# Performance work log

Measured on AMD Instinct MI355X. Metric: run time of the kernel, lower is better.

The kernel has to match this reference:

```python
import jax, jax.numpy as jnp
import numpy as np

H, C, DK = 4, 63, 64   # n_head, context_size, d_k
NF = H * DK            # n_feat = 256


def setup_inputs() -> dict:
    key = jax.random.key(0)
    ks = jax.random.split(key, 7)
    B, T = 2, 4096
    query = jax.random.normal(ks[0], (B, T, NF), jnp.float32)
    key_t = jax.random.normal(ks[1], (B, T, NF), jnp.float32)   # dummy, unused
    value = jax.random.normal(ks[2], (B, T, NF), jnp.float32)
    mask = jnp.ones((B, 1, T), jnp.bool_)                       # dummy, unused
    s = 1.0 / np.sqrt(NF).astype(np.float32)
    w1 = jax.random.normal(ks[3], (NF, NF), jnp.float32) * s
    w2 = jax.random.normal(ks[4], (H * C, NF), jnp.float32) * s
    w3 = jax.random.normal(ks[5], (NF, NF), jnp.float32) * s
    w_out = jax.random.normal(ks[6], (NF, NF), jnp.float32) * s
    return {"query": query, "key": key_t, "value": value, "mask": mask,
            "w1": w1, "w2": w2, "w3": w3, "w_out": w_out}


def reference(query, key, value, mask, w1, w2, w3, w_out):
    # key and mask are dummies (unused), matching the original module.
    B, T, _ = query.shape
    half = (C - 1) // 2

    q = query @ w1.T                                            # (B,T,NF)
    # synthesized band scores: (B,H,T,C)
    weight = (jax.nn.relu(q) @ w2.T).reshape(B, T, H, C).transpose(0, 2, 1, 3)

    # band geometry: score(i, j) lives at offset k = j - i + half, |j-i| <= half
    j_idx = jnp.arange(T)[:, None] + jnp.arange(C)[None, :] - half   # (T,C)
    valid = (j_idx >= 0) & (j_idx < T)                               # (T,C)
    scores = jnp.where(valid[None, None], weight, -jnp.inf)
    p_attn = jax.nn.softmax(scores, axis=-1)                         # (B,H,T,C)

    v = (value @ w3.T).reshape(B, T, H, DK).transpose(0, 2, 1, 3)    # (B,H,T,DK)
    jc = jnp.clip(j_idx, 0, T - 1)                                   # safe gather idx
    windows = v[:, :, jc, :]                                         # (B,H,T,C,DK)
    x = jnp.einsum('bhtc,bhtcd->bhtd', p_attn, windows)              # (B,H,T,DK)

    x = x.transpose(0, 2, 1, 3).reshape(B, T, NF)
    return x @ w_out.T
```

## Files before the change

### kernel.cpp

```cpp
#include <hip/hip_runtime.h>
#include <hip/hip_bf16.h>
#include <math.h>

typedef _Float16 f16x8 __attribute__((ext_vector_type(8)));
typedef _Float16 f16x4 __attribute__((ext_vector_type(4)));
typedef float    f32x4 __attribute__((ext_vector_type(4)));

__device__ __host__ __forceinline__ int swz(int ch, int row) {
    return (ch & 24) | ((ch & 7) ^ (row & 7));
}
__device__ __forceinline__ f32x4 mfma16(f16x8 a, f16x8 b, f32x4 c) {
    return __builtin_amdgcn_mfma_f32_16x16x32_f16(a, b, c, 0, 0, 0);
}
__device__ __forceinline__ f16x8 cvt8(float4 lo, float4 hi) {
    f16x8 r = { (_Float16)lo.x, (_Float16)lo.y, (_Float16)lo.z, (_Float16)lo.w,
                (_Float16)hi.x, (_Float16)hi.y, (_Float16)hi.z, (_Float16)hi.w };
    return r;
}

__global__ __launch_bounds__(256) void convw(const float* __restrict__ w1,
                                             const float* __restrict__ w2,
                                             const float* __restrict__ w3,
                                             const float* __restrict__ wo,
                                             _Float16* __restrict__ p1,
                                             _Float16* __restrict__ p2,
                                             _Float16* __restrict__ p3,
                                             _Float16* __restrict__ po) {
    int gid = blockIdx.x * 256 + threadIdx.x;
    int widx = gid >> 13;
    int r    = gid & 8191;
    int lane = r & 63;
    int ks   = (r >> 6) & 7;
    int nblk = r >> 9;
    int n  = nblk * 16 + (lane & 15);
    int kc = (ks * 4 + (lane >> 4)) * 8;
    const float* src = widx == 0 ? w1 : widx == 1 ? w2 : widx == 2 ? w3 : wo;
    _Float16*    dst = widx == 0 ? p1 : widx == 1 ? p2 : widx == 2 ? p3 : po;
    f16x8 h = {};
    if (!(widx == 1 && n >= 252)) {
        float4 lo = *(const float4*)&src[n * 256 + kc];
        float4 hi = *(const float4*)&src[n * 256 + kc + 4];
        h = cvt8(lo, hi);
    }
    *(f16x8*)&dst[r * 8] = h;
}

__global__ __launch_bounds__(1024) void mono(const float* __restrict__ query,
                                             const float* __restrict__ value,
                                             const _Float16* __restrict__ w1p,
                                             const _Float16* __restrict__ w2p,
                                             const _Float16* __restrict__ w3p,
                                             const _Float16* __restrict__ wop,
                                             float* __restrict__ outp) {
    __shared__ __align__(16) _Float16 RA[16384];
    __shared__ __align__(16) _Float16 RB[8192];
    __shared__ __align__(16) _Float16 Vs[24576];
    __shared__ __align__(16) _Float16 vwT[26624];

    const int tid = threadIdx.x, lane = tid & 63, wid = tid >> 6;
    const int bidr = blockIdx.x;
    const int work = (bidr & 7) * 32 + (bidr >> 3);
    const int b   = work >> 7;
    const int t0  = (work & 127) * 32;
    const size_t rowb = (size_t)b * 4096;

    _Float16* Aq = RA;
    _Float16* Qr = RA + 8192;
    _Float16* Pl = RA;
    _Float16* sc = RB;
    _Float16* xb = RB;

    {
        int row = tid >> 5, ch = tid & 31;
        const float* p = &query[(rowb + t0 + row) * 256 + ch * 8];
        float4 lo = *(const float4*)p, hi = *(const float4*)(p + 4);
        *(f16x8*)&Aq[row * 256 + swz(ch, row) * 8] = cvt8(lo, hi);
    }
    #pragma unroll
    for (int it = 0; it < 3; ++it) {
        int slot = it * 1024 + tid;
        int row = slot >> 5, ch = slot & 31;
        int jl = t0 - 32 + row;
        jl = jl < 0 ? 0 : (jl > 4095 ? 4095 : jl);
        const float* p = &value[(rowb + jl) * 256 + ch * 8];
        float4 lo = *(const float4*)p, hi = *(const float4*)(p + 4);
        *(f16x8*)&Vs[row * 256 + swz(ch, row) * 8] = cvt8(lo, hi);
    }
    __syncthreads();

    const int wm = wid >> 3;
    const int wn = wid & 7;

    {
        f32x4 acc[2] = {};
        #pragma unroll
        for (int ks = 0; ks < 8; ++ks) {
            int chn = ks * 4 + (lane >> 4);
            int row = wm * 16 + (lane & 15);
            f16x8 af = *(const f16x8*)&Aq[row * 256 + swz(chn, row) * 8];
            #pragma unroll
            for (int j = 0; j < 2; ++j) {
                f16x8 bf = *(const f16x8*)&w1p[(((wn * 2 + j) * 8 + ks) * 64 + lane) * 8];
                acc[j] = mfma16(af, bf, acc[j]);
            }
        }
        #pragma unroll
        for (int j = 0; j < 2; ++j)
            #pragma unroll
            for (int r = 0; r < 4; ++r) {
                int row = wm * 16 + ((lane >> 4) << 2) + r;
                int n   = wn * 32 + j * 16 + (lane & 15);
                float v = fmaxf(acc[j][r], 0.f);
                Qr[row * 256 + swz(n >> 3, row) * 8 + (n & 7)] = (_Float16)v;
            }
    }
    __syncthreads();

    {
        f32x4 acc[2] = {};
        #pragma unroll
        for (int ks = 0; ks < 8; ++ks) {
            int chn = ks * 4 + (lane >> 4);
            int row = wm * 16 + (lane & 15);
            f16x8 af = *(const f16x8*)&Qr[row * 256 + swz(chn, row) * 8];
            #pragma unroll
            for (int j = 0; j < 2; ++j) {
                f16x8 bf = *(const f16x8*)&w2p[(((wn * 2 + j) * 8 + ks) * 64 + lane) * 8];
                acc[j] = mfma16(af, bf, acc[j]);
            }
        }
        #pragma unroll
        for (int j = 0; j < 2; ++j)
            #pragma unroll
            for (int r = 0; r < 4; ++r) {
                int row = wm * 16 + ((lane >> 4) << 2) + r;
                int n   = wn * 32 + j * 16 + (lane & 15);
                sc[row * 256 + n] = (_Float16)acc[j][r];
            }
    }

    {
        f32x4 a3[3][2] = {};
        #pragma unroll
        for (int ks = 0; ks < 8; ++ks) {
            int chn = ks * 4 + (lane >> 4);
            f16x8 bf[2];
            #pragma unroll
            for (int j = 0; j < 2; ++j)
                bf[j] = *(const f16x8*)&w3p[(((wn * 2 + j) * 8 + ks) * 64 + lane) * 8];
            #pragma unroll
            for (int mi = 0; mi < 3; ++mi) {
                int row = (wm * 3 + mi) * 16 + (lane & 15);
                f16x8 af = *(const f16x8*)&Vs[row * 256 + swz(chn, row) * 8];
                #pragma unroll
                for (int j = 0; j < 2; ++j)
                    a3[mi][j] = mfma16(af, bf[j], a3[mi][j]);
            }
        }
        #pragma unroll
        for (int mi = 0; mi < 3; ++mi)
            #pragma unroll
            for (int j = 0; j < 2; ++j) {
                int d  = wn * 32 + j * 16 + (lane & 15);
                int jw = (wm * 3 + mi) * 16 + ((lane >> 4) << 2);
                f16x4 h = { (_Float16)a3[mi][j][0], (_Float16)a3[mi][j][1],
                            (_Float16)a3[mi][j][2], (_Float16)a3[mi][j][3] };
                *(f16x4*)&vwT[d * 104 + jw] = h;
            }
    }
    __syncthreads();

    const int h = wid >> 2, q = wid & 3;
    #pragma unroll
    for (int it = 0; it < 2; ++it) {
        int s = it * 64 + lane;
        if (s < 104) {
            int rr = h * 32 + q * 8 + s / 13;
            int cc = s % 13;
            f16x8 z = {};
            *(f16x8*)&Pl[rr * 104 + cc * 8] = z;
        }
    }

    {
        const int hf = lane >> 5, c = lane & 31;
        #pragma unroll
        for (int i = 0; i < 4; ++i) {
            int tl = q * 8 + 2 * i + hf;
            int t  = t0 + tl;
            int c1 = c + 32;
            int j0 = t + c - 31, j1 = t + c1 - 31;
            bool ok0 = (j0 >= 0) && (j0 < 4096);
            bool ok1 = (c1 < 63) && (j1 >= 0) && (j1 < 4096);
            float s0 = ok0 ? (float)sc[tl * 256 + h * 63 + c]  : -INFINITY;
            float s1 = ok1 ? (float)sc[tl * 256 + h * 63 + c1] : -INFINITY;
            float mx = fmaxf(s0, s1);
            #pragma unroll
            for (int off = 16; off > 0; off >>= 1) mx = fmaxf(mx, __shfl_xor(mx, off));
            float e0 = ok0 ? __expf(s0 - mx) : 0.f;
            float e1 = ok1 ? __expf(s1 - mx) : 0.f;
            float sum = e0 + e1;
            #pragma unroll
            for (int off = 16; off > 0; off >>= 1) sum += __shfl_xor(sum, off);
            float inv = 1.0f / sum;
            Pl[(h * 32 + tl) * 104 + (tl + c + 1)] = (_Float16)(e0 * inv);
            if (c1 < 63) Pl[(h * 32 + tl) * 104 + (tl + c1 + 1)] = (_Float16)(e1 * inv);
        }
    }
    __syncthreads();

    {
        const int th = (wid >> 1) & 1, dh = wid & 1;
        f32x4 xa[2] = {};
        #pragma unroll
        for (int ks = 0; ks < 3; ++ks) {
            int chn = ks * 4 + (lane >> 4);
            f16x8 af = *(const f16x8*)&Pl[(h * 32 + th * 16 + (lane & 15)) * 104 + chn * 8];
            #pragma unroll
            for (int j = 0; j < 2; ++j) {
                f16x8 bf = *(const f16x8*)&vwT[(h * 64 + dh * 32 + j * 16 + (lane & 15)) * 104 + chn * 8];
                xa[j] = mfma16(af, bf, xa[j]);
            }
        }
        #pragma unroll
        for (int j = 0; j < 2; ++j)
            #pragma unroll
            for (int r = 0; r < 4; ++r) {
                int row = th * 16 + ((lane >> 4) << 2) + r;
                int n   = h * 64 + dh * 32 + j * 16 + (lane & 15);
                xb[row * 256 + swz(n >> 3, row) * 8 + (n & 7)] = (_Float16)xa[j][r];
            }
    }
    __syncthreads();

    {
        f32x4 oa[2] = {};
        #pragma unroll
        for (int ks = 0; ks < 8; ++ks) {
            int chn = ks * 4 + (lane >> 4);
            int row = wm * 16 + (lane & 15);
            f16x8 af = *(const f16x8*)&xb[row * 256 + swz(chn, row) * 8];
            #pragma unroll
            for (int j = 0; j < 2; ++j) {
                f16x8 bf = *(const f16x8*)&wop[(((wn * 2 + j) * 8 + ks) * 64 + lane) * 8];
                oa[j] = mfma16(af, bf, oa[j]);
            }
        }
        #pragma unroll
        for (int j = 0; j < 2; ++j)
            #pragma unroll
            for (int r = 0; r < 4; ++r) {
                int m = t0 + wm * 16 + ((lane >> 4) << 2) + r;
                int n = wn * 32 + j * 16 + (lane & 15);
                outp[(rowb + m) * 256 + n] = oa[j][r];
            }
    }
}

extern "C" void kernel_launch(void* const* d_in, const int* in_sizes, int n_in,
                              void* d_out, int out_size, void* d_ws, size_t ws_size,
                              hipStream_t stream) {
    const float* query = (const float*)d_in[0];
    const float* value = (const float*)d_in[2];
    const float* w1    = (const float*)d_in[4];
    const float* w2    = (const float*)d_in[5];
    const float* w3    = (const float*)d_in[6];
    const float* w_out = (const float*)d_in[7];

    char* ws = (char*)d_ws;
    _Float16* w1p = (_Float16*)ws;
    _Float16* w2p = w1p + 65536;
    _Float16* w3p = w2p + 65536;
    _Float16* wop = w3p + 65536;

    convw<<<dim3(128), dim3(256), 0, stream>>>(w1, w2, w3, w_out, w1p, w2p, w3p, wop);
    mono<<<dim3(256), dim3(1024), 0, stream>>>(query, value, w1p, w2p, w3p, wop, (float*)d_out);
}
```

Baseline: 28.69 us.

## Repartition GEMM warps by output column and preload weight fragments

Each of the 16 waves now owns a 16-column slice of every GEMM's output across all rows, instead of a 2x8 grid of row and column tiles. Each wave therefore loads its weight fragments from global memory once into registers up front, and those fragments are reused across the row tiles. The global loads for query and value are all issued before their conversions and shared-memory stores, so the latency overlaps. Launch bounds now give a min-blocks hint, and the change raises register pressure from the eight preloaded fragments.

```diff
diff --git a/kernel.cpp b/kernel.cpp
--- a/kernel.cpp
+++ b/kernel.cpp
@@ -45,13 +45,13 @@
     *(f16x8*)&dst[r * 8] = h;
 }
 
-__global__ __launch_bounds__(1024) void mono(const float* __restrict__ query,
-                                             const float* __restrict__ value,
-                                             const _Float16* __restrict__ w1p,
-                                             const _Float16* __restrict__ w2p,
-                                             const _Float16* __restrict__ w3p,
-                                             const _Float16* __restrict__ wop,
-                                             float* __restrict__ outp) {
+__global__ __launch_bounds__(1024, 4) void mono(const float* __restrict__ query,
+                                                const float* __restrict__ value,
+                                                const _Float16* __restrict__ w1p,
+                                                const _Float16* __restrict__ w2p,
+                                                const _Float16* __restrict__ w3p,
+                                                const _Float16* __restrict__ wop,
+                                                float* __restrict__ outp) {
     __shared__ __align__(16) _Float16 RA[16384];
     __shared__ __align__(16) _Float16 RB[8192];
     __shared__ __align__(16) _Float16 Vs[24576];
@@ -72,101 +72,107 @@
 
     {
         int row = tid >> 5, ch = tid & 31;
-        const float* p = &query[(rowb + t0 + row) * 256 + ch * 8];
-        float4 lo = *(const float4*)p, hi = *(const float4*)(p + 4);
-        *(f16x8*)&Aq[row * 256 + swz(ch, row) * 8] = cvt8(lo, hi);
-    }
-    #pragma unroll
-    for (int it = 0; it < 3; ++it) {
-        int slot = it * 1024 + tid;
-        int row = slot >> 5, ch = slot & 31;
-        int jl = t0 - 32 + row;
-        jl = jl < 0 ? 0 : (jl > 4095 ? 4095 : jl);
-        const float* p = &value[(rowb + jl) * 256 + ch * 8];
-        float4 lo = *(const float4*)p, hi = *(const float4*)(p + 4);
-        *(f16x8*)&Vs[row * 256 + swz(ch, row) * 8] = cvt8(lo, hi);
-    }
-    __syncthreads();
-
-    const int wm = wid >> 3;
-    const int wn = wid & 7;
-
-    {
+        const float* qp = &query[(rowb + t0 + row) * 256 + ch * 8];
+        float4 qlo = *(const float4*)qp, qhi = *(const float4*)(qp + 4);
+        float4 vlo[3], vhi[3];
+        #pragma unroll
+        for (int it = 0; it < 3; ++it) {
+            int slot = it * 1024 + tid;
+            int vrow = slot >> 5, vch = slot & 31;
+            int jl = t0 - 32 + vrow;
+            jl = jl < 0 ? 0 : (jl > 4095 ? 4095 : jl);
+            const float* p = &value[(rowb + jl) * 256 + vch * 8];
+            vlo[it] = *(const float4*)p;
+            vhi[it] = *(const float4*)(p + 4);
+        }
+        *(f16x8*)&Aq[row * 256 + swz(ch, row) * 8] = cvt8(qlo, qhi);
+        #pragma unroll
+        for (int it = 0; it < 3; ++it) {
+            int slot = it * 1024 + tid;
+            int vrow = slot >> 5, vch = slot & 31;
+            *(f16x8*)&Vs[vrow * 256 + swz(vch, vrow) * 8] = cvt8(vlo[it], vhi[it]);
+        }
+    }
+    __syncthreads();
+
+    {
+        f16x8 bfa[8];
+        #pragma unroll
+        for (int ks = 0; ks < 8; ++ks)
+            bfa[ks] = *(const f16x8*)&w1p[((wid * 8 + ks) * 64 + lane) * 8];
         f32x4 acc[2] = {};
         #pragma unroll
         for (int ks = 0; ks < 8; ++ks) {
             int chn = ks * 4 + (lane >> 4);
-            int row = wm * 16 + (lane & 15);
-            f16x8 af = *(const f16x8*)&Aq[row * 256 + swz(chn, row) * 8];
-            #pragma unroll
-            for (int j = 0; j < 2; ++j) {
-                f16x8 bf = *(const f16x8*)&w1p[(((wn * 2 + j) * 8 + ks) * 64 + lane) * 8];
-                acc[j] = mfma16(af, bf, acc[j]);
-            }
-        }
-        #pragma unroll
-        for (int j = 0; j < 2; ++j)
-            #pragma unroll
-            for (int r = 0; r < 4; ++r) {
-                int row = wm * 16 + ((lane >> 4) << 2) + r;
-                int n   = wn * 32 + j * 16 + (lane & 15);
-                float v = fmaxf(acc[j][r], 0.f);
+            #pragma unroll
+            for (int i = 0; i < 2; ++i) {
+                int row = i * 16 + (lane & 15);
+                f16x8 af = *(const f16x8*)&Aq[row * 256 + swz(chn, row) * 8];
+                acc[i] = mfma16(af, bfa[ks], acc[i]);
+            }
+        }
+        const int n = wid * 16 + (lane & 15);
+        #pragma unroll
+        for (int i = 0; i < 2; ++i)
+            #pragma unroll
+            for (int r = 0; r < 4; ++r) {
+                int row = i * 16 + ((lane >> 4) << 2) + r;
+                float v = fmaxf(acc[i][r], 0.f);
                 Qr[row * 256 + swz(n >> 3, row) * 8 + (n & 7)] = (_Float16)v;
             }
     }
     __syncthreads();
 
     {
+        f16x8 bfa[8];
+        #pragma unroll
+        for (int ks = 0; ks < 8; ++ks)
+            bfa[ks] = *(const f16x8*)&w2p[((wid * 8 + ks) * 64 + lane) * 8];
         f32x4 acc[2] = {};
         #pragma unroll
         for (int ks = 0; ks < 8; ++ks) {
             int chn = ks * 4 + (lane >> 4);
-            int row = wm * 16 + (lane & 15);
-            f16x8 af = *(const f16x8*)&Qr[row * 256 + swz(chn, row) * 8];
-            #pragma unroll
-            for (int j = 0; j < 2; ++j) {
-                f16x8 bf = *(const f16x8*)&w2p[(((wn * 2 + j) * 8 + ks) * 64 + lane) * 8];
-                acc[j] = mfma16(af, bf, acc[j]);
-            }
-        }
-        #pragma unroll
-        for (int j = 0; j < 2; ++j)
-            #pragma unroll
-            for (int r = 0; r < 4; ++r) {
-                int row = wm * 16 + ((lane >> 4) << 2) + r;
-                int n   = wn * 32 + j * 16 + (lane & 15);
-                sc[row * 256 + n] = (_Float16)acc[j][r];
-            }
-    }
-
-    {
-        f32x4 a3[3][2] = {};
-        #pragma unroll
-        for (int ks = 0; ks < 8; ++ks) {
-            int chn = ks * 4 + (lane >> 4);
-            f16x8 bf[2];
-            #pragma unroll
-            for (int j = 0; j < 2; ++j)
-                bf[j] = *(const f16x8*)&w3p[(((wn * 2 + j) * 8 + ks) * 64 + lane) * 8];
-            #pragma unroll
-            for (int mi = 0; mi < 3; ++mi) {
-                int row = (wm * 3 + mi) * 16 + (lane & 15);
+            #pragma unroll
+            for (int i = 0; i < 2; ++i) {
+                int row = i * 16 + (lane & 15);
+                f16x8 af = *(const f16x8*)&Qr[row * 256 + swz(chn, row) * 8];
+                acc[i] = mfma16(af, bfa[ks], acc[i]);
+            }
+        }
+        const int n = wid * 16 + (lane & 15);
+        #pragma unroll
+        for (int i = 0; i < 2; ++i)
+            #pragma unroll
+            for (int r = 0; r < 4; ++r) {
+                int row = i * 16 + ((lane >> 4) << 2) + r;
+                sc[row * 256 + n] = (_Float16)acc[i][r];
+            }
+    }
+
+    {
+        f16x8 bfa[8];
+        #pragma unroll
+        for (int ks = 0; ks < 8; ++ks)
+            bfa[ks] = *(const f16x8*)&w3p[((wid * 8 + ks) * 64 + lane) * 8];
+        f32x4 a3[6] = {};
+        #pragma unroll
+        for (int ks = 0; ks < 8; ++ks) {
+            int chn = ks * 4 + (lane >> 4);
+            #pragma unroll
+            for (int mi = 0; mi < 6; ++mi) {
+                int row = mi * 16 + (lane & 15);
                 f16x8 af = *(const f16x8*)&Vs[row * 256 + swz(chn, row) * 8];
-                #pragma unroll
-                for (int j = 0; j < 2; ++j)
-                    a3[mi][j] = mfma16(af, bf[j], a3[mi][j]);
-            }
-        }
-        #pragma unroll
-        for (int mi = 0; mi < 3; ++mi)
-            #pragma unroll
-            for (int j = 0; j < 2; ++j) {
-                int d  = wn * 32 + j * 16 + (lane & 15);
-                int jw = (wm * 3 + mi) * 16 + ((lane >> 4) << 2);
-                f16x4 h = { (_Float16)a3[mi][j][0], (_Float16)a3[mi][j][1],
-                            (_Float16)a3[mi][j][2], (_Float16)a3[mi][j][3] };
-                *(f16x4*)&vwT[d * 104 + jw] = h;
-            }
+                a3[mi] = mfma16(af, bfa[ks], a3[mi]);
+            }
+        }
+        const int d = wid * 16 + (lane & 15);
+        #pragma unroll
+        for (int mi = 0; mi < 6; ++mi) {
+            int jw = mi * 16 + ((lane >> 4) << 2);
+            f16x4 h = { (_Float16)a3[mi][0], (_Float16)a3[mi][1],
+                        (_Float16)a3[mi][2], (_Float16)a3[mi][3] };
+            *(f16x4*)&vwT[d * 104 + jw] = h;
+        }
     }
     __syncthreads();
 
@@ -234,25 +240,28 @@
     __syncthreads();
 
     {
+        f16x8 bfa[8];
+        #pragma unroll
+        for (int ks = 0; ks < 8; ++ks)
+            bfa[ks] = *(const f16x8*)&wop[((wid * 8 + ks) * 64 + lane) * 8];
         f32x4 oa[2] = {};
         #pragma unroll
         for (int ks = 0; ks < 8; ++ks) {
             int chn = ks * 4 + (lane >> 4);
-            int row = wm * 16 + (lane & 15);
-            f16x8 af = *(const f16x8*)&xb[row * 256 + swz(chn, row) * 8];
-            #pragma unroll
-            for (int j = 0; j < 2; ++j) {
-                f16x8 bf = *(const f16x8*)&wop[(((wn * 2 + j) * 8 + ks) * 64 + lane) * 8];
-                oa[j] = mfma16(af, bf, oa[j]);
-            }
-        }
-        #pragma unroll
-        for (int j = 0; j < 2; ++j)
-            #pragma unroll
-            for (int r = 0; r < 4; ++r) {
-                int m = t0 + wm * 16 + ((lane >> 4) << 2) + r;
-                int n = wn * 32 + j * 16 + (lane & 15);
-                outp[(rowb + m) * 256 + n] = oa[j][r];
+            #pragma unroll
+            for (int i = 0; i < 2; ++i) {
+                int row = i * 16 + (lane & 15);
+                f16x8 af = *(const f16x8*)&xb[row * 256 + swz(chn, row) * 8];
+                oa[i] = mfma16(af, bfa[ks], oa[i]);
+            }
+        }
+        const int n = wid * 16 + (lane & 15);
+        #pragma unroll
+        for (int i = 0; i < 2; ++i)
+            #pragma unroll
+            for (int r = 0; r < 4; ++r) {
+                int m = t0 + i * 16 + ((lane >> 4) << 2) + r;
+                outp[(rowb + m) * 256 + n] = oa[i][r];
             }
     }
 }
```

Result: faster. 25.63 us (-10.7%).
